# Kernel optimization log

Measured on AMD Instinct MI355X. Metric: run time of the kernel, lower is better.

## Reference

```python
import jax, jax.numpy as jnp
import numpy as np

B = 1024      # batch
D_NUM = 100   # numeric features
N_CAT = 20    # categorical features
CARD = 100    # cardinality per categorical feature
D = 1024      # d_token
DH = 675      # int(d_token * 0.66)
NT = D_NUM + 1 + N_CAT  # 121 tokens (CLS + numeric + categorical)
E = 4         # num_experts
K = 2         # top_k
MID = 512     # ResidualHead mid dim = max(D//2, 16)
RH = 256      # router/alpha hidden = max(D//4, 16)


def _ln(x, g, b):
    m = x.mean(-1, keepdims=True)
    v = ((x - m) ** 2).mean(-1, keepdims=True)
    return (x - m) * jax.lax.rsqrt(v + 1e-5) * g + b


def setup_inputs() -> dict:
    key = jax.random.key(0)
    ks = jax.random.split(key, 20)

    def n(i, shape, s=0.02):
        return jax.random.normal(ks[i], shape, dtype=jnp.float32) * s

    return dict(
        x_num=jax.random.normal(ks[0], (B, D_NUM), dtype=jnp.float32),
        x_cat=jax.random.randint(ks[1], (B, N_CAT), 0, CARD),
        tok_w=n(2, (D_NUM + 1, D), 0.05),
        tok_b=n(3, (D_NUM + N_CAT, D), 0.05),
        cat_emb=n(4, (N_CAT * CARD, D), 0.05),
        ln_g=jnp.ones((D,), jnp.float32), ln_b=jnp.zeros((D,), jnp.float32),
        lin0_w=n(5, (D, 2 * DH)), lin0_b=jnp.zeros((2 * DH,), jnp.float32),
        sgu_ln_g=jnp.ones((DH,), jnp.float32), sgu_ln_b=jnp.zeros((DH,), jnp.float32),
        sgu_w=n(6, (NT, NT), 0.05), sgu_b=jnp.zeros((NT,), jnp.float32),
        lin1_w=n(7, (DH, D)), lin1_b=jnp.zeros((D,), jnp.float32),
        r_w1=n(8, (D, RH)), r_b1=jnp.zeros((RH,), jnp.float32),
        r_w2=n(9, (RH, E)), r_b2=jnp.zeros((E,), jnp.float32),
        a_w1=n(10, (D, RH)), a_b1=jnp.zeros((RH,), jnp.float32),
        a_w2=n(11, (RH, 1)), a_b2=jnp.full((1,), -4.0, jnp.float32),
        base_w=n(12, (D, 1)), base_b=jnp.zeros((1,), jnp.float32),
        gh_w1=n(13, (D, MID), 0.001), gh_b1=jnp.zeros((MID,), jnp.float32),
        gh_w2=n(14, (MID, 1), 0.001), gh_b2=jnp.zeros((1,), jnp.float32),
        ex_w1=n(15, (E, D, MID), 0.001), ex_b1=jnp.zeros((E, MID), jnp.float32),
        ex_w2=n(16, (E, MID), 0.001), ex_b2=jnp.zeros((E,), jnp.float32),
    )


def reference(x_num, x_cat, tok_w, tok_b, cat_emb, ln_g, ln_b, lin0_w, lin0_b,
              sgu_ln_g, sgu_ln_b, sgu_w, sgu_b, lin1_w, lin1_b,
              r_w1, r_b1, r_w2, r_b2, a_w1, a_b1, a_w2, a_b2,
              base_w, base_b, gh_w1, gh_b1, gh_w2, gh_b2,
              ex_w1, ex_b1, ex_w2, ex_b2):
    # ---- Tokenizer ----
    offsets = jnp.arange(N_CAT) * CARD
    xn = jnp.concatenate([jnp.ones((x_num.shape[0], 1), x_num.dtype), x_num], axis=1)  # [B, D_NUM+1]
    x = tok_w[None] * xn[:, :, None]                                  # [B, D_NUM+1, D]
    x = jnp.concatenate([x, cat_emb[x_cat + offsets[None]]], axis=1)  # [B, NT, D]
    bias_full = jnp.concatenate([jnp.zeros((1, D), tok_b.dtype), tok_b], axis=0)
    x = x + bias_full[None]
    # ---- gMLP layer (n_layers=1) ----
    xr = x
    h = _ln(x, ln_g, ln_b)
    h = jax.nn.gelu(h @ lin0_w + lin0_b, approximate=False)           # [B, NT, 2*DH]
    u, v = h[..., :DH], h[..., DH:]
    v = _ln(v, sgu_ln_g, sgu_ln_b)
    # SGU token-mixing: out[b,s,d] = sum_t v[b,t,d] * W[s,t] + bias[s]
    v = jnp.einsum('btd,st->bsd', v, sgu_w) + sgu_b[None, :, None]
    x = (u * v) @ lin1_w + lin1_b
    x = x + xr
    # ---- pooled hidden (CLS token) ----
    hidden = jax.nn.gelu(_ln(x[:, 0], ln_g, ln_b), approximate=False)  # [B, D]
    # ---- router + top-k sparsification ----
    logits = jax.nn.relu(hidden @ r_w1 + r_b1) @ r_w2 + r_b2           # [B, E]
    dense = jax.nn.softmax(logits, axis=-1)
    vals, idx = jax.lax.top_k(dense, K)
    sparse = jnp.zeros_like(dense).at[jnp.arange(dense.shape[0])[:, None], idx].set(vals)
    rw = sparse / jnp.clip(sparse.sum(-1, keepdims=True), 1e-8)
    # ---- local experts (small residual heads, vectorized over E) ----
    eh = jax.nn.relu(jnp.einsum('bd,edm->bem', hidden, ex_w1) + ex_b1[None])
    eo = jnp.einsum('bem,em->be', eh, ex_w2) + ex_b2[None]             # [B, E]
    local = (rw * eo).sum(-1, keepdims=True)                           # [B, 1]
    # ---- global residual, alpha gate, base head ----
    glob = jax.nn.relu(hidden @ gh_w1 + gh_b1) @ gh_w2 + gh_b2
    alpha = jax.nn.sigmoid(jax.nn.relu(hidden @ a_w1 + a_b1) @ a_w2 + a_b2)
    y_base = hidden @ base_w + base_b
    return y_base + alpha * (glob + local)                             # [B, 1]
```

## Files before the change

kernel.cpp:

```cpp
#include <hip/hip_runtime.h>
#include <math.h>

#define B_SZ 1024

typedef __attribute__((ext_vector_type(8))) short bf16x8;
typedef __attribute__((ext_vector_type(4))) float f32x4;
typedef __attribute__((ext_vector_type(4))) float floatx4;
typedef __attribute__((ext_vector_type(4))) unsigned short ushortx4;

#define GLOAD16(src, dst) __builtin_amdgcn_global_load_lds( \
    (const __attribute__((address_space(1))) void*)(src), \
    (__attribute__((address_space(3))) void*)(dst), 16, 0, 0)

__device__ __forceinline__ unsigned short f2bf(float f) {
  unsigned int u = __float_as_uint(f);
  u += 0x7fff + ((u >> 16) & 1);
  return (unsigned short)(u >> 16);
}
__device__ __forceinline__ float bf2f(unsigned short b) {
  return __uint_as_float(((unsigned int)b) << 16);
}
__device__ __forceinline__ float gelu_exact(float x) {
  return 0.5f * x * (1.0f + erff(x * 0.70710678118654752f));
}
__device__ __forceinline__ float gelu_fast(float x) {
  const float c0 = 2.3022586f;
  const float c1 = 0.10295465f;
  float z = x * __builtin_fmaf(x * x, c1, c0);
  float e = __builtin_amdgcn_exp2f(z);
  float r = __builtin_amdgcn_rcpf(e + 1.0f);
  return __builtin_fmaf(-x, r, x);
}
__device__ __forceinline__ float wred(float v) {
#pragma unroll
  for (int o = 32; o > 0; o >>= 1) v += __shfl_xor(v, o, 64);
  return v;
}

struct PrepArgs {
  const float* src[10];
  unsigned short* dst[10];
  int ldin[10]; int coff[10]; int Nsrc[10]; int Ksrc[10]; int Kp[10];
  int nbx[10]; int blk0[11];
};

__global__ __launch_bounds__(256)
void prep_all(PrepArgs J,
              const float* __restrict__ tok_w, const float* __restrict__ tok_b,
              const float* __restrict__ cat_emb,
              const float* __restrict__ ln_g, const float* __restrict__ ln_b,
              const float* __restrict__ r_b1, const float* __restrict__ a_b1,
              const float* __restrict__ gh_b1, const float* __restrict__ ex_b1,
              unsigned short* __restrict__ Amat,
              float* __restrict__ nstat, float* __restrict__ cstat,
              float* __restrict__ bcat)
{
  const int bid = blockIdx.x;
  const int tid = threadIdx.x;
  const int lane = tid & 63;
  const int NT = J.blk0[10];
  if (bid < NT) {
    __shared__ float tile[64][65];
    int j = 0;
    while (bid >= J.blk0[j + 1]) ++j;
    const int bx = bid - J.blk0[j];
    const int k0 = (bx % J.nbx[j]) * 64;
    const int n0 = (bx / J.nbx[j]) * 64;
    const float* in = J.src[j];
    unsigned short* out = J.dst[j];
    const int ldin = J.ldin[j], coff = J.coff[j], Nsrc = J.Nsrc[j], Ksrc = J.Ksrc[j], Kp = J.Kp[j];
    const int kx = tid & 63;
    const int ry = tid >> 6;
    for (int r = ry; r < 64; r += 4) {
      const int k = k0 + r;
      const int n = n0 + kx;
      tile[r][kx] = (k < Ksrc && n < Nsrc) ? in[(size_t)k * ldin + coff + n] : 0.f;
    }
    __syncthreads();
    for (int r = ry; r < 64; r += 4) {
      const int n = n0 + r;
      const int k = k0 + kx;
      out[(size_t)n * Kp + k] = f2bf(tile[kx][r]);
    }
  } else if (bid < NT + 576) {
    const int r = (bid - NT) * 4 + (tid >> 6);
    if (r >= 2304) return;
    unsigned short* out = Amat + (size_t)r * 1024;
    for (int k = lane * 4; k < 1024; k += 256) {
      floatx4 g = *(const floatx4*)(ln_g + k);
      floatx4 v;
      if (r <= 100) {
        floatx4 a = *(const floatx4*)(tok_w + (size_t)r * 1024 + k);
#pragma unroll
        for (int q = 0; q < 4; q++) v[q] = a[q] * g[q];
      } else if (r <= 200) {
        floatx4 a = *(const floatx4*)(tok_b + (size_t)(r - 101) * 1024 + k);
#pragma unroll
        for (int q = 0; q < 4; q++) v[q] = a[q] * g[q];
      } else if (r <= 2200) {
        const int j = r - 201;
        const int c = j / 100;
        floatx4 a = *(const floatx4*)(cat_emb + (size_t)j * 1024 + k);
        floatx4 bq = *(const floatx4*)(tok_b + (size_t)(100 + c) * 1024 + k);
#pragma unroll
        for (int q = 0; q < 4; q++) v[q] = (a[q] + bq[q]) * g[q];
      } else if (r == 2201) {
        v = g;
      } else if (r == 2202) {
        v = *(const floatx4*)(ln_b + k);
      } else {
        v[0] = 0.f; v[1] = 0.f; v[2] = 0.f; v[3] = 0.f;
      }
      ushortx4 o;
#pragma unroll
      for (int q = 0; q < 4; q++) o[q] = f2bf(v[q]);
      *(ushortx4*)(out + k) = o;
    }
  } else if (bid < NT + 576 + 526) {
    const int w = (bid - NT - 576) * 4 + (tid >> 6);
    if (w >= 2101) return;
    if (w <= 100) {
      const int t = w;
      const float* wr = tok_w + (size_t)t * 1024;
      const float* br = (t >= 1) ? (tok_b + (size_t)(t - 1) * 1024) : nullptr;
      float sw = 0, sww = 0, sb = 0, sbb = 0, swb = 0;
      for (int k = lane * 4; k < 1024; k += 256) {
        floatx4 a = *(const floatx4*)(wr + k);
#pragma unroll
        for (int q = 0; q < 4; q++) { sw += a[q]; sww += a[q] * a[q]; }
        if (br) {
          floatx4 bq = *(const floatx4*)(br + k);
#pragma unroll
          for (int q = 0; q < 4; q++) { sb += bq[q]; sbb += bq[q] * bq[q]; swb += a[q] * bq[q]; }
        }
      }
      sw = wred(sw); sww = wred(sww); sb = wred(sb); sbb = wred(sbb); swb = wred(swb);
      if (lane == 0) {
        float* ns = nstat + (size_t)t * 5;
        ns[0] = sw; ns[1] = sww; ns[2] = sb; ns[3] = sbb; ns[4] = swb;
      }
    } else {
      const int j = w - 101;
      const int c = j / 100;
      const float* ar = cat_emb + (size_t)j * 1024;
      const float* br = tok_b + (size_t)(100 + c) * 1024;
      float s1 = 0, s2 = 0;
      for (int k = lane * 4; k < 1024; k += 256) {
        floatx4 a = *(const floatx4*)(ar + k);
        floatx4 bq = *(const floatx4*)(br + k);
#pragma unroll
        for (int q = 0; q < 4; q++) { const float v = a[q] + bq[q]; s1 += v; s2 += v * v; }
      }
      s1 = wred(s1); s2 = wred(s2);
      if (lane == 0) { cstat[(size_t)j * 2] = s1; cstat[(size_t)j * 2 + 1] = s2; }
    }
  } else {
    const int n = (bid - NT - 1102) * 256 + tid;
    if (n >= 3072) return;
    float v;
    if (n < 256) v = r_b1[n];
    else if (n < 512) v = a_b1[n - 256];
    else if (n < 1024) v = gh_b1[n - 512];
    else v = ex_b1[n - 1024];
    bcat[n] = v;
  }
}

template<int EPI>
__device__ __forceinline__
void gemm_body(int bid, const unsigned short* __restrict__ A, long pitchA,
               const unsigned short* __restrict__ Bw, int K,
               const float* __restrict__ bias, int bias_off,
               const float* __restrict__ extra,
               int NB, int Nvalid, int ldo,
               float* __restrict__ outf, unsigned short* __restrict__ outb)
{
  __shared__ unsigned short As[128 * 32];
  __shared__ unsigned short Bs[128 * 32];
  const int tid = threadIdx.x, lane = tid & 63, wv = tid >> 6;
  const int nb = bid % NB, mb = bid / NB;
  const int m0 = mb * 128, n0 = nb * 128;
  const int wr = (wv >> 1) << 6, wc = (wv & 1) << 6;
  const int fr = lane & 15, fq = lane >> 4;
  const int c0 = wv * 2;
  const int srow = lane >> 2;
  const int sk = (lane & 3) << 3;

  const unsigned short* a0 = A + (size_t)(m0 + c0 * 16 + srow) * pitchA + sk;
  const unsigned short* a1 = A + (size_t)(m0 + (c0 + 1) * 16 + srow) * pitchA + sk;
  const unsigned short* b0p = Bw + (size_t)(n0 + c0 * 16 + srow) * K + sk;
  const unsigned short* b1p = Bw + (size_t)(n0 + (c0 + 1) * 16 + srow) * K + sk;

  f32x4 acc[4][4] = {};
  for (int k0 = 0; k0 < K; k0 += 32) {
    __syncthreads();
    GLOAD16(a0 + k0, &As[c0 * 512]);
    GLOAD16(a1 + k0, &As[(c0 + 1) * 512]);
    GLOAD16(b0p + k0, &Bs[c0 * 512]);
    GLOAD16(b1p + k0, &Bs[(c0 + 1) * 512]);
    __syncthreads();
    bf16x8 af[4], bw_[4];
#pragma unroll
    for (int i = 0; i < 4; i++) {
      af[i]  = *(const bf16x8*)&As[(wr + i * 16 + fr) * 32 + fq * 8];
      bw_[i] = *(const bf16x8*)&Bs[(wc + i * 16 + fr) * 32 + fq * 8];
    }
#pragma unroll
    for (int i = 0; i < 4; i++)
#pragma unroll
      for (int j = 0; j < 4; j++)
        acc[i][j] = __builtin_amdgcn_mfma_f32_16x16x32_bf16(af[i], bw_[j], acc[i][j], 0, 0, 0);
  }

#pragma unroll
  for (int i = 0; i < 4; i++)
#pragma unroll
    for (int j = 0; j < 4; j++) {
      const int n = n0 + wc + j * 16 + fr;
      if (n >= ldo) continue;
      const bool valid = (n < Nvalid);
      const float bv = (EPI == 3) ? 0.f : (valid ? bias[bias_off + n] : 0.f);
      const float ev = (EPI == 0) ? extra[n] : 0.f;
#pragma unroll
      for (int q = 0; q < 4; q++) {
        const int m = m0 + wr + i * 16 + fq * 4 + q;
        const float a = acc[i][j][q];
        if (EPI == 0) {
          outf[(size_t)m * ldo + n] = a + bv + ev;
        } else if (EPI == 1) {
          outb[(size_t)m * ldo + n] = f2bf(fmaxf(a + bv, 0.f));
        } else {
          outf[(size_t)m * ldo + n] = a;
        }
      }
    }
}

template<int EPI>
__global__ __launch_bounds__(256)
void gemm_gl(const unsigned short* __restrict__ A, long pitchA,
             const unsigned short* __restrict__ Bw, int K,
             const float* __restrict__ bias, int bias_off,
             const float* __restrict__ extra,
             int NB, int Nvalid, int ldo,
             float* __restrict__ outf, unsigned short* __restrict__ outb)
{
  gemm_body<EPI>(blockIdx.x, A, pitchA, Bw, K, bias, bias_off, extra, NB, Nvalid, ldo, outf, outb);
}

__device__ __forceinline__
void u_const_body(int bid, const unsigned short* __restrict__ w0u, const float* __restrict__ nstat,
                  const float* __restrict__ tok_w, const float* __restrict__ ln_g,
                  const float* __restrict__ ln_b, const float* __restrict__ lin0_b,
                  float* __restrict__ ucon)
{
  __shared__ float xk[1024];
  const int tid = threadIdx.x, lane = tid & 63, wv = tid >> 6;
  const float m = nstat[0] * (1.f / 1024.f);
  const float ex2 = nstat[1] * (1.f / 1024.f);
  const float rs = rsqrtf(ex2 - m * m + 1e-5f);
  for (int k = tid; k < 1024; k += 256)
    xk[k] = bf2f(f2bf((tok_w[k] - m) * rs * ln_g[k] + ln_b[k]));
  __syncthreads();
  const int c = bid * 4 + wv;
  if (c >= 704) return;
  if (c >= 675) { if (lane == 0) ucon[c] = 0.f; return; }
  const unsigned short* wr = w0u + (size_t)c * 1024;
  float s = 0.f;
  for (int k = lane; k < 1024; k += 64) s += bf2f(wr[k]) * xk[k];
  s = wred(s);
  if (lane == 0) ucon[c] = gelu_exact(s + lin0_b[c]);
}

__global__ __launch_bounds__(256)
void tab_and_u(const unsigned short* __restrict__ Amat, const unsigned short* __restrict__ w0v,
               float* __restrict__ TAB,
               const unsigned short* __restrict__ w0u, const float* __restrict__ nstat,
               const float* __restrict__ tok_w, const float* __restrict__ ln_g,
               const float* __restrict__ ln_b, const float* __restrict__ lin0_b,
               float* __restrict__ ucon)
{
  if (blockIdx.x < 108)
    gemm_body<3>(blockIdx.x, Amat, 1024, w0v, 1024, nullptr, 0, nullptr, 6, 768, 768, TAB, nullptr);
  else
    u_const_body(blockIdx.x - 108, w0u, nstat, tok_w, ln_g, ln_b, lin0_b, ucon);
}

__global__ __launch_bounds__(256)
void cat_rows(const float* __restrict__ TAB, const float* __restrict__ nstat,
              const float* __restrict__ cstat, const float* __restrict__ lin0_b,
              float* __restrict__ catval, float* __restrict__ catsc)
{
  const int r = blockIdx.x * 4 + (threadIdx.x >> 6);
  const int lane = threadIdx.x & 63;
  if (r >= 2001) return;
  float m, ex2;
  const float* T1;
  if (r < 2000) {
    m = cstat[(size_t)r * 2] * (1.f / 1024.f);
    ex2 = cstat[(size_t)r * 2 + 1] * (1.f / 1024.f);
    T1 = TAB + (size_t)(201 + r) * 768;
  } else {
    m = nstat[0] * (1.f / 1024.f);
    ex2 = nstat[1] * (1.f / 1024.f);
    T1 = TAB;
  }
  const float rs = rsqrtf(ex2 - m * m + 1e-5f);
  const float ga = -m * rs;
  const float* R = TAB + (size_t)2201 * 768;
  const float* C = TAB + (size_t)2202 * 768;
  const int dl = lane << 2;
  float s = 0.f, ss = 0.f;
  float* outp = catval + (size_t)r * 768;
#pragma unroll
  for (int ch = 0; ch < 3; ch++) {
    const int d = ch * 256 + dl;
    floatx4 t1 = *(const floatx4*)(T1 + d);
    floatx4 rr = *(const floatx4*)(R + d);
    floatx4 cc = *(const floatx4*)(C + d);
    floatx4 o;
#pragma unroll
    for (int q = 0; q < 4; q++) {
      const int dd = d + q;
      const float c2 = (dd < 675) ? (cc[q] + lin0_b[675 + dd]) : 0.f;
      const float pre = __builtin_fmaf(rs, t1[q], __builtin_fmaf(ga, rr[q], c2));
      const float g = (dd < 675) ? gelu_fast(pre) : 0.f;
      o[q] = g; s += g; ss = __builtin_fmaf(g, g, ss);
    }
    *(floatx4*)(outp + d) = o;
  }
  s = wred(s); ss = wred(ss);
  const float mu = s * (1.f / 675.f);
  const float rho = rsqrtf(ss * (1.f / 675.f) - mu * mu + 1e-5f);
  if (lane == 0) { catsc[(size_t)r * 2] = mu; catsc[(size_t)r * 2 + 1] = rho; }
}

__global__ __launch_bounds__(512)
void fused_v2(const float* __restrict__ TAB, const float* __restrict__ nstat,
              const float* __restrict__ catsc, const float* __restrict__ catval,
              const float* __restrict__ x_num, const int* __restrict__ x_cat,
              const float* __restrict__ sgu_ln_g, const float* __restrict__ sgu_ln_b,
              const float* __restrict__ sgu_w, const float* __restrict__ sgu_b,
              const float* __restrict__ lin0_b, const float* __restrict__ ucon,
              unsigned short* __restrict__ uv)
{
  const int b0 = blockIdx.x, b1 = blockIdx.x + 512;
  const int tid = threadIdx.x, lane = tid & 63, wv = tid >> 6;
  __shared__ float Rls[768], Cls[768];
  __shared__ float alf[2][100], bet[2][100], gam[2][100], swt[100];
  __shared__ float wrc[2][21], catkb[2][21];
  __shared__ int catrowS[2][21];
  __shared__ float accw[8][768];
  __shared__ float kbw[2][8];
  __shared__ float wss_s;

  for (int d = tid; d < 768; d += 512) {
    Rls[d] = (d < 675) ? TAB[(size_t)2201 * 768 + d] : 0.f;
    Cls[d] = (d < 675) ? (TAB[(size_t)2202 * 768 + d] + lin0_b[675 + d]) : 0.f;
  }
  if (tid < 200) {
    const int bb = tid / 100, tt = tid % 100;
    const int b = bb ? b1 : b0;
    const float sc = x_num[b * 100 + tt];
    const float* ns = nstat + (size_t)(tt + 1) * 5;
    const float m = (sc * ns[0] + ns[2]) * (1.f / 1024.f);
    const float ex2 = (sc * sc * ns[1] + 2.f * sc * ns[4] + ns[3]) * (1.f / 1024.f);
    const float rs = rsqrtf(ex2 - m * m + 1e-5f);
    alf[bb][tt] = rs * sc; bet[bb][tt] = rs; gam[bb][tt] = -m * rs;
    if (bb == 0) swt[tt] = sgu_w[tt + 1];
  } else if (tid < 242) {
    const int idx = tid - 200;
    const int bb = idx / 21, ii = idx % 21;
    const int b = bb ? b1 : b0;
    int row; float sw;
    if (ii < 20) { row = x_cat[b * 20 + ii] + 100 * ii; sw = sgu_w[101 + ii]; }
    else { row = 2000; sw = sgu_w[0]; }
    const float mu = catsc[(size_t)row * 2], rho = catsc[(size_t)row * 2 + 1];
    const float wr = sw * rho;
    wrc[bb][ii] = wr; catkb[bb][ii] = wr * mu; catrowS[bb][ii] = row;
  } else if (tid >= 256 && tid < 320) {
    float s = (lane < 121 ? sgu_w[lane] : 0.f) + (lane + 64 < 121 ? sgu_w[lane + 64] : 0.f);
    s = wred(s);
    if (lane == 0) wss_s = s;
  }
  __syncthreads();

  float accA[12] = {}, accB[12] = {};
  float kbA = 0.f, kbB = 0.f;
  const int dl = lane << 2;

  for (int i = 0; i < 13; i++) {
    const int tt = wv + 8 * i;
    if (tt >= 100) break;
    const float a0 = alf[0][tt], be0 = bet[0][tt], ga0 = gam[0][tt];
    const float a1 = alf[1][tt], be1 = bet[1][tt], ga1 = gam[1][tt];
    const float* T1 = TAB + (size_t)(tt + 1) * 768;
    const float* T2 = TAB + (size_t)(101 + tt) * 768;
    float s0 = 0.f, ss0 = 0.f, s1 = 0.f, ss1 = 0.f;
    float va[12], vb[12];
#pragma unroll
    for (int ch = 0; ch < 3; ch++) {
      const int d = ch * 256 + dl;
      floatx4 t1 = *(const floatx4*)(T1 + d);
      floatx4 t2 = *(const floatx4*)(T2 + d);
      floatx4 rr = *(const floatx4*)(&Rls[d]);
      floatx4 cc = *(const floatx4*)(&Cls[d]);
#pragma unroll
      for (int q = 0; q < 4; q++) {
        const float pre0 = __builtin_fmaf(a0, t1[q], __builtin_fmaf(be0, t2[q], __builtin_fmaf(ga0, rr[q], cc[q])));
        const float g0 = gelu_fast(pre0);
        va[ch * 4 + q] = g0; s0 += g0; ss0 = __builtin_fmaf(g0, g0, ss0);
        const float pre1 = __builtin_fmaf(a1, t1[q], __builtin_fmaf(be1, t2[q], __builtin_fmaf(ga1, rr[q], cc[q])));
        const float g1 = gelu_fast(pre1);
        vb[ch * 4 + q] = g1; s1 += g1; ss1 = __builtin_fmaf(g1, g1, ss1);
      }
    }
    s0 = wred(s0); ss0 = wred(ss0); s1 = wred(s1); ss1 = wred(ss1);
    const float sw = swt[tt];
    const float mu0 = s0 * (1.f / 675.f);
    const float rho0 = rsqrtf(ss0 * (1.f / 675.f) - mu0 * mu0 + 1e-5f);
    const float w0 = sw * rho0;
    const float mu1 = s1 * (1.f / 675.f);
    const float rho1 = rsqrtf(ss1 * (1.f / 675.f) - mu1 * mu1 + 1e-5f);
    const float w1 = sw * rho1;
#pragma unroll
    for (int q = 0; q < 12; q++) {
      accA[q] = __builtin_fmaf(w0, va[q], accA[q]);
      accB[q] = __builtin_fmaf(w1, vb[q], accB[q]);
    }
    kbA = __builtin_fmaf(w0, mu0, kbA);
    kbB = __builtin_fmaf(w1, mu1, kbB);
  }

  for (int i = 0; i < 3; i++) {
    const int ii = wv + 8 * i;
    if (ii >= 21) break;
    {
      const float wr = wrc[0][ii];
      const float* cv = catval + (size_t)catrowS[0][ii] * 768;
#pragma unroll
      for (int ch = 0; ch < 3; ch++) {
        floatx4 v = *(const floatx4*)(cv + ch * 256 + dl);
#pragma unroll
        for (int q = 0; q < 4; q++) accA[ch * 4 + q] = __builtin_fmaf(wr, v[q], accA[ch * 4 + q]);
      }
    }
    {
      const float wr = wrc[1][ii];
      const float* cv = catval + (size_t)catrowS[1][ii] * 768;
#pragma unroll
      for (int ch = 0; ch < 3; ch++) {
        floatx4 v = *(const floatx4*)(cv + ch * 256 + dl);
#pragma unroll
        for (int q = 0; q < 4; q++) accB[ch * 4 + q] = __builtin_fmaf(wr, v[q], accB[ch * 4 + q]);
      }
    }
  }
  if (lane == 0) { kbw[0][wv] = kbA; kbw[1][wv] = kbB; }

  const float sb0 = sgu_b[0];

#pragma unroll
  for (int ch = 0; ch < 3; ch++)
    *(floatx4*)&accw[wv][ch * 256 + dl] = *(const floatx4*)&accA[ch * 4];
  __syncthreads();
  {
    float kbs = 0.f;
#pragma unroll
    for (int w = 0; w < 8; w++) kbs += kbw[0][w];
#pragma unroll
    for (int i = 0; i < 21; i++) kbs += catkb[0][i];
    const float wss = wss_s;
    for (int d = tid; d < 704; d += 512) {
      unsigned short o = 0;
      if (d < 675) {
        float a = 0.f;
#pragma unroll
        for (int w = 0; w < 8; w++) a += accw[w][d];
        const float v0 = sgu_ln_g[d] * (a - kbs) + sgu_ln_b[d] * wss + sb0;
        o = f2bf(ucon[d] * v0);
      }
      uv[(size_t)b0 * 704 + d] = o;
    }
  }
  __syncthreads();
#pragma unroll
  for (int ch = 0; ch < 3; ch++)
    *(floatx4*)&accw[wv][ch * 256 + dl] = *(const floatx4*)&accB[ch * 4];
  __syncthreads();
  {
    float kbs = 0.f;
#pragma unroll
    for (int w = 0; w < 8; w++) kbs += kbw[1][w];
#pragma unroll
    for (int i = 0; i < 21; i++) kbs += catkb[1][i];
    const float wss = wss_s;
    for (int d = tid; d < 704; d += 512) {
      unsigned short o = 0;
      if (d < 675) {
        float a = 0.f;
#pragma unroll
        for (int w = 0; w < 8; w++) a += accw[w][d];
        const float v0 = sgu_ln_g[d] * (a - kbs) + sgu_ln_b[d] * wss + sb0;
        o = f2bf(ucon[d] * v0);
      }
      uv[(size_t)b1 * 704 + d] = o;
    }
  }
}

__global__ __launch_bounds__(256)
void ln_gelu_hidden(const float* __restrict__ xfin,
                    const float* __restrict__ ln_g, const float* __restrict__ ln_b,
                    float* __restrict__ hid_f, unsigned short* __restrict__ hid_bf)
{
  const int w = (blockIdx.x * 256 + threadIdx.x) >> 6;
  const int lane = threadIdx.x & 63;
  if (w >= B_SZ) return;
  const float* row = xfin + (size_t)w * 1024;
  float s = 0.f, ss = 0.f;
  for (int k = lane; k < 1024; k += 64) { float v = row[k]; s += v; ss += v * v; }
  s = wred(s); ss = wred(ss);
  const float m = s * (1.f / 1024.f);
  const float var = ss * (1.f / 1024.f) - m * m;
  const float rs = rsqrtf(var + 1e-5f);
  for (int k = lane; k < 1024; k += 64) {
    float v = gelu_exact((row[k] - m) * rs * ln_g[k] + ln_b[k]);
    hid_f[(size_t)w * 1024 + k] = v;
    hid_bf[(size_t)w * 1024 + k] = f2bf(v);
  }
}

__global__ __launch_bounds__(256)
void final_head(const unsigned short* __restrict__ H1, const float* __restrict__ hid_f,
                const float* __restrict__ r_w2, const float* __restrict__ r_b2,
                const float* __restrict__ a_w2, const float* __restrict__ a_b2,
                const float* __restrict__ gh_w2, const float* __restrict__ gh_b2,
                const float* __restrict__ ex_w2, const float* __restrict__ ex_b2,
                const float* __restrict__ base_w, const float* __restrict__ base_b,
                float* __restrict__ out)
{
  const int b = blockIdx.x;
  const int tid = threadIdx.x;
  const unsigned short* h1 = H1 + (size_t)b * 3072;
  float p[11];
#pragma unroll
  for (int i = 0; i < 11; i++) p[i] = 0.f;
  {
    const int m = tid;
    const float hr = bf2f(h1[m]);
    p[0] = hr * r_w2[m * 4 + 0];
    p[1] = hr * r_w2[m * 4 + 1];
    p[2] = hr * r_w2[m * 4 + 2];
    p[3] = hr * r_w2[m * 4 + 3];
    const float ha = bf2f(h1[256 + m]);
    p[4] = ha * a_w2[m];
  }
  for (int m = tid; m < 512; m += 256) {
    p[5] += bf2f(h1[512 + m]) * gh_w2[m];
#pragma unroll
    for (int e = 0; e < 4; e++)
      p[6 + e] += bf2f(h1[1024 + e * 512 + m]) * ex_w2[e * 512 + m];
  }
  for (int k = tid; k < 1024; k += 256) p[10] += hid_f[(size_t)b * 1024 + k] * base_w[k];

  __shared__ float red[11][4];
  const int lane = tid & 63, wv = tid >> 6;
#pragma unroll
  for (int i = 0; i < 11; i++) {
    const float v = wred(p[i]);
    if (lane == 0) red[i][wv] = v;
  }
  __syncthreads();
  if (tid == 0) {
    float s[11];
#pragma unroll
    for (int i = 0; i < 11; i++) s[i] = red[i][0] + red[i][1] + red[i][2] + red[i][3];
    float lg[4];
#pragma unroll
    for (int e = 0; e < 4; e++) lg[e] = s[e] + r_b2[e];
    const float mx = fmaxf(fmaxf(lg[0], lg[1]), fmaxf(lg[2], lg[3]));
    float den[4]; float dsum = 0.f;
#pragma unroll
    for (int e = 0; e < 4; e++) { den[e] = expf(lg[e] - mx); dsum += den[e]; }
#pragma unroll
    for (int e = 0; e < 4; e++) den[e] /= dsum;
    int i1 = 0;
    for (int e = 1; e < 4; e++) if (den[e] > den[i1]) i1 = e;
    int i2 = -1;
    for (int e = 0; e < 4; e++) { if (e == i1) continue; if (i2 < 0 || den[e] > den[i2]) i2 = e; }
    float eo[4];
#pragma unroll
    for (int e = 0; e < 4; e++) eo[e] = s[6 + e] + ex_b2[e];
    const float v1 = den[i1], v2 = den[i2];
    const float ssum = fmaxf(v1 + v2, 1e-8f);
    const float local = (v1 * eo[i1] + v2 * eo[i2]) / ssum;
    const float glob = s[5] + gh_b2[0];
    const float alpha = 1.0f / (1.0f + expf(-(s[4] + a_b2[0])));
    out[b] = s[10] + base_b[0] + alpha * (glob + local);
  }
}

extern "C" void kernel_launch(void* const* d_in, const int* in_sizes, int n_in,
                              void* d_out, int out_size, void* d_ws, size_t ws_size,
                              hipStream_t stream)
{
  const float* x_num  = (const float*)d_in[0];
  const int*   x_cat  = (const int*)d_in[1];
  const float* tok_w  = (const float*)d_in[2];
  const float* tok_b  = (const float*)d_in[3];
  const float* cat_emb= (const float*)d_in[4];
  const float* ln_g   = (const float*)d_in[5];
  const float* ln_b   = (const float*)d_in[6];
  const float* lin0_w = (const float*)d_in[7];
  const float* lin0_b = (const float*)d_in[8];
  const float* sgu_ln_g = (const float*)d_in[9];
  const float* sgu_ln_b = (const float*)d_in[10];
  const float* sgu_w  = (const float*)d_in[11];
  const float* sgu_b  = (const float*)d_in[12];
  const float* lin1_w = (const float*)d_in[13];
  const float* lin1_b = (const float*)d_in[14];
  const float* r_w1   = (const float*)d_in[15];
  const float* r_b1   = (const float*)d_in[16];
  const float* r_w2   = (const float*)d_in[17];
  const float* r_b2   = (const float*)d_in[18];
  const float* a_w1   = (const float*)d_in[19];
  const float* a_b1   = (const float*)d_in[20];
  const float* a_w2   = (const float*)d_in[21];
  const float* a_b2   = (const float*)d_in[22];
  const float* base_w = (const float*)d_in[23];
  const float* base_b = (const float*)d_in[24];
  const float* gh_w1  = (const float*)d_in[25];
  const float* gh_b1  = (const float*)d_in[26];
  const float* gh_w2  = (const float*)d_in[27];
  const float* gh_b2  = (const float*)d_in[28];
  const float* ex_w1  = (const float*)d_in[29];
  const float* ex_b1  = (const float*)d_in[30];
  const float* ex_w2  = (const float*)d_in[31];
  const float* ex_b2  = (const float*)d_in[32];
  (void)in_sizes; (void)n_in; (void)out_size; (void)ws_size;

  char* ws = (char*)d_ws;
  size_t off = 0;
  auto alloc = [&](size_t bytes) { void* p = ws + off; off += (bytes + 255) & ~(size_t)255; return p; };

  unsigned short* w0v  = (unsigned short*)alloc((size_t)768 * 1024 * 2);
  unsigned short* w0u  = (unsigned short*)alloc((size_t)768 * 1024 * 2);
  unsigned short* w1t  = (unsigned short*)alloc((size_t)1024 * 704 * 2);
  unsigned short* wcat = (unsigned short*)alloc((size_t)3072 * 1024 * 2);
  float* bcat          = (float*)alloc((size_t)3072 * 4);
  unsigned short* Amat = (unsigned short*)alloc((size_t)2304 * 1024 * 2);
  float* TAB           = (float*)alloc((size_t)2304 * 768 * 4);
  float* nstat         = (float*)alloc((size_t)101 * 5 * 4);
  float* cstat         = (float*)alloc((size_t)2000 * 2 * 4);
  float* catval        = (float*)alloc((size_t)2001 * 768 * 4);
  float* catsc         = (float*)alloc((size_t)2001 * 2 * 4);
  float* ucon          = (float*)alloc((size_t)704 * 4);
  unsigned short* uv   = (unsigned short*)alloc((size_t)B_SZ * 704 * 2);
  float* xfin          = (float*)alloc((size_t)B_SZ * 1024 * 4);
  float* hid_f         = (float*)alloc((size_t)B_SZ * 1024 * 4);
  unsigned short* hidb = (unsigned short*)alloc((size_t)B_SZ * 1024 * 2);
  unsigned short* H1   = (unsigned short*)alloc((size_t)B_SZ * 3072 * 2);

  const dim3 blk(256);

  PrepArgs J;
  auto setJ = [&](int i, const float* s, unsigned short* d, int ldin, int coff,
                  int Nsrc, int Ksrc, int Kp, int nbx, int nby) {
    J.src[i] = s; J.dst[i] = d; J.ldin[i] = ldin; J.coff[i] = coff;
    J.Nsrc[i] = Nsrc; J.Ksrc[i] = Ksrc; J.Kp[i] = Kp; J.nbx[i] = nbx;
    J.blk0[i + 1] = J.blk0[i] + nbx * nby;
  };
  J.blk0[0] = 0;
  setJ(0, lin0_w, w0v, 1350, 675, 675, 1024, 1024, 16, 12);
  setJ(1, lin0_w, w0u, 1350, 0,   675, 1024, 1024, 16, 12);
  setJ(2, lin1_w, w1t, 1024, 0,  1024,  675,  704, 11, 16);
  setJ(3, r_w1,  wcat,                          256, 0, 256, 1024, 1024, 16, 4);
  setJ(4, a_w1,  wcat + (size_t)256 * 1024,     256, 0, 256, 1024, 1024, 16, 4);
  setJ(5, gh_w1, wcat + (size_t)512 * 1024,     512, 0, 512, 1024, 1024, 16, 8);
  for (int e = 0; e < 4; e++)
    setJ(6 + e, ex_w1 + (size_t)e * 1024 * 512,
         wcat + (size_t)(1024 + e * 512) * 1024, 512, 0, 512, 1024, 1024, 16, 8);

  const int nprep = J.blk0[10] + 576 + 526 + 12;
  prep_all<<<nprep, blk, 0, stream>>>(J, tok_w, tok_b, cat_emb, ln_g, ln_b,
      r_b1, a_b1, gh_b1, ex_b1, Amat, nstat, cstat, bcat);

  tab_and_u<<<284, blk, 0, stream>>>(Amat, w0v, TAB, w0u, nstat, tok_w, ln_g, ln_b, lin0_b, ucon);

  cat_rows<<<501, blk, 0, stream>>>(TAB, nstat, cstat, lin0_b, catval, catsc);

  fused_v2<<<512, dim3(512), 0, stream>>>(TAB, nstat, catsc, catval, x_num, x_cat,
      sgu_ln_g, sgu_ln_b, sgu_w, sgu_b, lin0_b, ucon, uv);

  gemm_gl<0><<<8 * 8, blk, 0, stream>>>(uv, 704, w1t, 704,
      lin1_b, 0, tok_w, 8, 1024, 1024, xfin, nullptr);
  ln_gelu_hidden<<<B_SZ / 4, blk, 0, stream>>>(xfin, ln_g, ln_b, hid_f, hidb);
  gemm_gl<1><<<8 * 24, blk, 0, stream>>>(hidb, 1024, wcat, 1024,
      bcat, 0, nullptr, 24, 3072, 3072, nullptr, H1);

  final_head<<<B_SZ, blk, 0, stream>>>(H1, hid_f, r_w2, r_b2, a_w2, a_b2, gh_w2, gh_b2,
                                       ex_w2, ex_b2, base_w, base_b, (float*)d_out);
}
```

Measured before the change: 152.1 us.

## Fuse base head into LN-GELU, unroll fused token loop by two, hoist sgu sum

The base-head dot product moves into the LN+GELU kernel, so the fp32 hidden buffer is no longer written or re-read by final_head. The fused token loop now handles two tokens per iteration for more memory-level parallelism, with a launch-bounds occupancy hint added. The per-block sgu_w sum is computed once in cat_rows instead of in every block. The hidden GELU also switches from exact erf to the fast approximation, which may change accuracy.

Result: slower. 161.3 us (+6.1%).

```diff
diff --git a/kernel.cpp b/kernel.cpp
--- a/kernel.cpp
+++ b/kernel.cpp
@@ -289,11 +289,20 @@
 __global__ __launch_bounds__(256)
 void cat_rows(const float* __restrict__ TAB, const float* __restrict__ nstat,
               const float* __restrict__ cstat, const float* __restrict__ lin0_b,
-              float* __restrict__ catval, float* __restrict__ catsc)
+              const float* __restrict__ sgu_w,
+              float* __restrict__ catval, float* __restrict__ catsc,
+              float* __restrict__ wss_g)
 {
   const int r = blockIdx.x * 4 + (threadIdx.x >> 6);
   const int lane = threadIdx.x & 63;
-  if (r >= 2001) return;
+  if (r == 2001) {
+    float s = (lane < 121) ? sgu_w[lane] : 0.f;
+    if (lane + 64 < 121) s += sgu_w[lane + 64];
+    s = wred(s);
+    if (lane == 0) wss_g[0] = s;
+    return;
+  }
+  if (r > 2001) return;
   float m, ex2;
   const float* T1;
   if (r < 2000) {
@@ -335,13 +344,14 @@
   if (lane == 0) { catsc[(size_t)r * 2] = mu; catsc[(size_t)r * 2 + 1] = rho; }
 }
 
-__global__ __launch_bounds__(512)
-void fused_v2(const float* __restrict__ TAB, const float* __restrict__ nstat,
+__global__ __launch_bounds__(512, 4)
+void fused_v3(const float* __restrict__ TAB, const float* __restrict__ nstat,
               const float* __restrict__ catsc, const float* __restrict__ catval,
               const float* __restrict__ x_num, const int* __restrict__ x_cat,
               const float* __restrict__ sgu_ln_g, const float* __restrict__ sgu_ln_b,
               const float* __restrict__ sgu_w, const float* __restrict__ sgu_b,
               const float* __restrict__ lin0_b, const float* __restrict__ ucon,
+              const float* __restrict__ wss_g,
               unsigned short* __restrict__ uv)
 {
   const int b0 = blockIdx.x, b1 = blockIdx.x + 512;
@@ -352,7 +362,6 @@
   __shared__ int catrowS[2][21];
   __shared__ float accw[8][768];
   __shared__ float kbw[2][8];
-  __shared__ float wss_s;
 
   for (int d = tid; d < 768; d += 512) {
     Rls[d] = (d < 675) ? TAB[(size_t)2201 * 768 + d] : 0.f;
@@ -378,10 +387,6 @@
     const float mu = catsc[(size_t)row * 2], rho = catsc[(size_t)row * 2 + 1];
     const float wr = sw * rho;
     wrc[bb][ii] = wr; catkb[bb][ii] = wr * mu; catrowS[bb][ii] = row;
-  } else if (tid >= 256 && tid < 320) {
-    float s = (lane < 121 ? sgu_w[lane] : 0.f) + (lane + 64 < 121 ? sgu_w[lane + 64] : 0.f);
-    s = wred(s);
-    if (lane == 0) wss_s = s;
   }
   __syncthreads();
 
@@ -389,47 +394,64 @@
   float kbA = 0.f, kbB = 0.f;
   const int dl = lane << 2;
 
-  for (int i = 0; i < 13; i++) {
-    const int tt = wv + 8 * i;
-    if (tt >= 100) break;
-    const float a0 = alf[0][tt], be0 = bet[0][tt], ga0 = gam[0][tt];
-    const float a1 = alf[1][tt], be1 = bet[1][tt], ga1 = gam[1][tt];
-    const float* T1 = TAB + (size_t)(tt + 1) * 768;
-    const float* T2 = TAB + (size_t)(101 + tt) * 768;
-    float s0 = 0.f, ss0 = 0.f, s1 = 0.f, ss1 = 0.f;
-    float va[12], vb[12];
+  for (int i = 0; i < 7; i++) {
+    const int tA = wv + 16 * i;
+    if (tA >= 100) break;
+    const int tB = tA + 8;
+    const bool hB = (tB < 100);
+    const int tBs = hB ? tB : tA;
+    const float aA0 = alf[0][tA], eA0 = bet[0][tA], gA0 = gam[0][tA];
+    const float aA1 = alf[1][tA], eA1 = bet[1][tA], gA1 = gam[1][tA];
+    const float aB0 = alf[0][tBs], eB0 = bet[0][tBs], gB0 = gam[0][tBs];
+    const float aB1 = alf[1][tBs], eB1 = bet[1][tBs], gB1 = gam[1][tBs];
+    const float* T1A = TAB + (size_t)(tA + 1) * 768;
+    const float* T2A = TAB + (size_t)(101 + tA) * 768;
+    const float* T1B = TAB + (size_t)(tBs + 1) * 768;
+    const float* T2B = TAB + (size_t)(101 + tBs) * 768;
+    float vA0[12], vA1[12], vB0[12], vB1[12];
+    float sA0 = 0.f, qA0 = 0.f, sA1 = 0.f, qA1 = 0.f;
+    float sB0 = 0.f, qB0 = 0.f, sB1 = 0.f, qB1 = 0.f;
 #pragma unroll
     for (int ch = 0; ch < 3; ch++) {
       const int d = ch * 256 + dl;
-      floatx4 t1 = *(const floatx4*)(T1 + d);
-      floatx4 t2 = *(const floatx4*)(T2 + d);
+      floatx4 t1a = *(const floatx4*)(T1A + d);
+      floatx4 t2a = *(const floatx4*)(T2A + d);
+      floatx4 t1b = *(const floatx4*)(T1B + d);
+      floatx4 t2b = *(const floatx4*)(T2B + d);
       floatx4 rr = *(const floatx4*)(&Rls[d]);
       floatx4 cc = *(const floatx4*)(&Cls[d]);
 #pragma unroll
       for (int q = 0; q < 4; q++) {
-        const float pre0 = __builtin_fmaf(a0, t1[q], __builtin_fmaf(be0, t2[q], __builtin_fmaf(ga0, rr[q], cc[q])));
-        const float g0 = gelu_fast(pre0);
-        va[ch * 4 + q] = g0; s0 += g0; ss0 = __builtin_fmaf(g0, g0, ss0);
-        const float pre1 = __builtin_fmaf(a1, t1[q], __builtin_fmaf(be1, t2[q], __builtin_fmaf(ga1, rr[q], cc[q])));
-        const float g1 = gelu_fast(pre1);
-        vb[ch * 4 + q] = g1; s1 += g1; ss1 = __builtin_fmaf(g1, g1, ss1);
-      }
-    }
-    s0 = wred(s0); ss0 = wred(ss0); s1 = wred(s1); ss1 = wred(ss1);
-    const float sw = swt[tt];
-    const float mu0 = s0 * (1.f / 675.f);
-    const float rho0 = rsqrtf(ss0 * (1.f / 675.f) - mu0 * mu0 + 1e-5f);
-    const float w0 = sw * rho0;
-    const float mu1 = s1 * (1.f / 675.f);
-    const float rho1 = rsqrtf(ss1 * (1.f / 675.f) - mu1 * mu1 + 1e-5f);
-    const float w1 = sw * rho1;
+        const float bcA = __builtin_fmaf(gA0, rr[q], cc[q]);
+        const float g0 = gelu_fast(__builtin_fmaf(aA0, t1a[q], __builtin_fmaf(eA0, t2a[q], bcA)));
+        vA0[ch * 4 + q] = g0; sA0 += g0; qA0 = __builtin_fmaf(g0, g0, qA0);
+        const float g1 = gelu_fast(__builtin_fmaf(aA1, t1a[q], __builtin_fmaf(eA1, t2a[q], __builtin_fmaf(gA1, rr[q], cc[q]))));
+        vA1[ch * 4 + q] = g1; sA1 += g1; qA1 = __builtin_fmaf(g1, g1, qA1);
+        const float g2 = gelu_fast(__builtin_fmaf(aB0, t1b[q], __builtin_fmaf(eB0, t2b[q], __builtin_fmaf(gB0, rr[q], cc[q]))));
+        vB0[ch * 4 + q] = g2; sB0 += g2; qB0 = __builtin_fmaf(g2, g2, qB0);
+        const float g3 = gelu_fast(__builtin_fmaf(aB1, t1b[q], __builtin_fmaf(eB1, t2b[q], __builtin_fmaf(gB1, rr[q], cc[q]))));
+        vB1[ch * 4 + q] = g3; sB1 += g3; qB1 = __builtin_fmaf(g3, g3, qB1);
+      }
+    }
+    sA0 = wred(sA0); qA0 = wred(qA0); sA1 = wred(sA1); qA1 = wred(qA1);
+    sB0 = wred(sB0); qB0 = wred(qB0); sB1 = wred(sB1); qB1 = wred(qB1);
+    const float swA = swt[tA];
+    const float swB = hB ? swt[tBs] : 0.f;
+    const float muA0 = sA0 * (1.f / 675.f);
+    const float wA0 = swA * rsqrtf(qA0 * (1.f / 675.f) - muA0 * muA0 + 1e-5f);
+    const float muA1 = sA1 * (1.f / 675.f);
+    const float wA1 = swA * rsqrtf(qA1 * (1.f / 675.f) - muA1 * muA1 + 1e-5f);
+    const float muB0 = sB0 * (1.f / 675.f);
+    const float wB0 = swB * rsqrtf(qB0 * (1.f / 675.f) - muB0 * muB0 + 1e-5f);
+    const float muB1 = sB1 * (1.f / 675.f);
+    const float wB1 = swB * rsqrtf(qB1 * (1.f / 675.f) - muB1 * muB1 + 1e-5f);
 #pragma unroll
     for (int q = 0; q < 12; q++) {
-      accA[q] = __builtin_fmaf(w0, va[q], accA[q]);
-      accB[q] = __builtin_fmaf(w1, vb[q], accB[q]);
-    }
-    kbA = __builtin_fmaf(w0, mu0, kbA);
-    kbB = __builtin_fmaf(w1, mu1, kbB);
+      accA[q] = __builtin_fmaf(wA0, vA0[q], __builtin_fmaf(wB0, vB0[q], accA[q]));
+      accB[q] = __builtin_fmaf(wA1, vA1[q], __builtin_fmaf(wB1, vB1[q], accB[q]));
+    }
+    kbA = __builtin_fmaf(wA0, muA0, __builtin_fmaf(wB0, muB0, kbA));
+    kbB = __builtin_fmaf(wA1, muA1, __builtin_fmaf(wB1, muB1, kbB));
   }
 
   for (int i = 0; i < 3; i++) {
@@ -459,6 +481,7 @@
   if (lane == 0) { kbw[0][wv] = kbA; kbw[1][wv] = kbB; }
 
   const float sb0 = sgu_b[0];
+  const float wss = wss_g[0];
 
 #pragma unroll
   for (int ch = 0; ch < 3; ch++)
@@ -470,7 +493,6 @@
     for (int w = 0; w < 8; w++) kbs += kbw[0][w];
 #pragma unroll
     for (int i = 0; i < 21; i++) kbs += catkb[0][i];
-    const float wss = wss_s;
     for (int d = tid; d < 704; d += 512) {
       unsigned short o = 0;
       if (d < 675) {
@@ -494,7 +516,6 @@
     for (int w = 0; w < 8; w++) kbs += kbw[1][w];
 #pragma unroll
     for (int i = 0; i < 21; i++) kbs += catkb[1][i];
-    const float wss = wss_s;
     for (int d = tid; d < 704; d += 512) {
       unsigned short o = 0;
       if (d < 675) {
@@ -512,7 +533,8 @@
 __global__ __launch_bounds__(256)
 void ln_gelu_hidden(const float* __restrict__ xfin,
                     const float* __restrict__ ln_g, const float* __restrict__ ln_b,
-                    float* __restrict__ hid_f, unsigned short* __restrict__ hid_bf)
+                    const float* __restrict__ base_w,
+                    unsigned short* __restrict__ hid_bf, float* __restrict__ base_y)
 {
   const int w = (blockIdx.x * 256 + threadIdx.x) >> 6;
   const int lane = threadIdx.x & 63;
@@ -524,28 +546,31 @@
   const float m = s * (1.f / 1024.f);
   const float var = ss * (1.f / 1024.f) - m * m;
   const float rs = rsqrtf(var + 1e-5f);
+  float bacc = 0.f;
   for (int k = lane; k < 1024; k += 64) {
-    float v = gelu_exact((row[k] - m) * rs * ln_g[k] + ln_b[k]);
-    hid_f[(size_t)w * 1024 + k] = v;
+    float v = gelu_fast((row[k] - m) * rs * ln_g[k] + ln_b[k]);
     hid_bf[(size_t)w * 1024 + k] = f2bf(v);
-  }
+    bacc = __builtin_fmaf(v, base_w[k], bacc);
+  }
+  bacc = wred(bacc);
+  if (lane == 0) base_y[w] = bacc;
 }
 
 __global__ __launch_bounds__(256)
-void final_head(const unsigned short* __restrict__ H1, const float* __restrict__ hid_f,
+void final_head(const unsigned short* __restrict__ H1, const float* __restrict__ base_y,
                 const float* __restrict__ r_w2, const float* __restrict__ r_b2,
                 const float* __restrict__ a_w2, const float* __restrict__ a_b2,
                 const float* __restrict__ gh_w2, const float* __restrict__ gh_b2,
                 const float* __restrict__ ex_w2, const float* __restrict__ ex_b2,
-                const float* __restrict__ base_w, const float* __restrict__ base_b,
+                const float* __restrict__ base_b,
                 float* __restrict__ out)
 {
   const int b = blockIdx.x;
   const int tid = threadIdx.x;
   const unsigned short* h1 = H1 + (size_t)b * 3072;
-  float p[11];
-#pragma unroll
-  for (int i = 0; i < 11; i++) p[i] = 0.f;
+  float p[10];
+#pragma unroll
+  for (int i = 0; i < 10; i++) p[i] = 0.f;
   {
     const int m = tid;
     const float hr = bf2f(h1[m]);
@@ -562,20 +587,19 @@
     for (int e = 0; e < 4; e++)
       p[6 + e] += bf2f(h1[1024 + e * 512 + m]) * ex_w2[e * 512 + m];
   }
-  for (int k = tid; k < 1024; k += 256) p[10] += hid_f[(size_t)b * 1024 + k] * base_w[k];
-
-  __shared__ float red[11][4];
+
+  __shared__ float red[10][4];
   const int lane = tid & 63, wv = tid >> 6;
 #pragma unroll
-  for (int i = 0; i < 11; i++) {
+  for (int i = 0; i < 10; i++) {
     const float v = wred(p[i]);
     if (lane == 0) red[i][wv] = v;
   }
   __syncthreads();
   if (tid == 0) {
-    float s[11];
-#pragma unroll
-    for (int i = 0; i < 11; i++) s[i] = red[i][0] + red[i][1] + red[i][2] + red[i][3];
+    float s[10];
+#pragma unroll
+    for (int i = 0; i < 10; i++) s[i] = red[i][0] + red[i][1] + red[i][2] + red[i][3];
     float lg[4];
 #pragma unroll
     for (int e = 0; e < 4; e++) lg[e] = s[e] + r_b2[e];
@@ -597,7 +621,7 @@
     const float local = (v1 * eo[i1] + v2 * eo[i2]) / ssum;
     const float glob = s[5] + gh_b2[0];
     const float alpha = 1.0f / (1.0f + expf(-(s[4] + a_b2[0])));
-    out[b] = s[10] + base_b[0] + alpha * (glob + local);
+    out[b] = base_y[b] + base_b[0] + alpha * (glob + local);
   }
 }
 
@@ -656,9 +680,10 @@
   float* catval        = (float*)alloc((size_t)2001 * 768 * 4);
   float* catsc         = (float*)alloc((size_t)2001 * 2 * 4);
   float* ucon          = (float*)alloc((size_t)704 * 4);
+  float* wss_g         = (float*)alloc((size_t)4);
   unsigned short* uv   = (unsigned short*)alloc((size_t)B_SZ * 704 * 2);
   float* xfin          = (float*)alloc((size_t)B_SZ * 1024 * 4);
-  float* hid_f         = (float*)alloc((size_t)B_SZ * 1024 * 4);
+  float* base_y        = (float*)alloc((size_t)B_SZ * 4);
   unsigned short* hidb = (unsigned short*)alloc((size_t)B_SZ * 1024 * 2);
   unsigned short* H1   = (unsigned short*)alloc((size_t)B_SZ * 3072 * 2);
 
@@ -688,17 +713,17 @@
 
   tab_and_u<<<284, blk, 0, stream>>>(Amat, w0v, TAB, w0u, nstat, tok_w, ln_g, ln_b, lin0_b, ucon);
 
-  cat_rows<<<501, blk, 0, stream>>>(TAB, nstat, cstat, lin0_b, catval, catsc);
-
-  fused_v2<<<512, dim3(512), 0, stream>>>(TAB, nstat, catsc, catval, x_num, x_cat,
-      sgu_ln_g, sgu_ln_b, sgu_w, sgu_b, lin0_b, ucon, uv);
+  cat_rows<<<501, blk, 0, stream>>>(TAB, nstat, cstat, lin0_b, sgu_w, catval, catsc, wss_g);
+
+  fused_v3<<<512, dim3(512), 0, stream>>>(TAB, nstat, catsc, catval, x_num, x_cat,
+      sgu_ln_g, sgu_ln_b, sgu_w, sgu_b, lin0_b, ucon, wss_g, uv);
 
   gemm_gl<0><<<8 * 8, blk, 0, stream>>>(uv, 704, w1t, 704,
       lin1_b, 0, tok_w, 8, 1024, 1024, xfin, nullptr);
-  ln_gelu_hidden<<<B_SZ / 4, blk, 0, stream>>>(xfin, ln_g, ln_b, hid_f, hidb);
+  ln_gelu_hidden<<<B_SZ / 4, blk, 0, stream>>>(xfin, ln_g, ln_b, base_w, hidb, base_y);
   gemm_gl<1><<<8 * 24, blk, 0, stream>>>(hidb, 1024, wcat, 1024,
       bcat, 0, nullptr, 24, 3072, 3072, nullptr, H1);
 
-  final_head<<<B_SZ, blk, 0, stream>>>(H1, hid_f, r_w2, r_b2, a_w2, a_b2, gh_w2, gh_b2,
-                                       ex_w2, ex_b2, base_w, base_b, (float*)d_out);
-}
+  final_head<<<B_SZ, blk, 0, stream>>>(H1, base_y, r_w2, r_b2, a_w2, a_b2, gh_w2, gh_b2,
+                                       ex_w2, ex_b2, base_b, (float*)d_out);
+}
```
